# Kernel tuning notes

Measured on AMD Instinct MI355X. Metric: run time of the kernel, lower is better.

Reference implementation:

```python
import jax, jax.numpy as jnp
import numpy as np

N, D, K = 100000, 512, 32
H1, H2 = 512, 256
LN2PI_2 = float(np.log(2.0 * np.pi) / 2.0)


def _glorot(key, shape):
    fan_in, fan_out = shape[0], shape[1]
    limit = np.sqrt(6.0 / (fan_in + fan_out))
    return jax.random.uniform(key, shape, jnp.float32, -limit, limit)


def setup_inputs() -> dict:
    key = jax.random.key(0)
    k0, k1, k2, k3 = jax.random.split(key, 4)
    return {
        "x": jax.random.normal(k0, (N, D), jnp.float32),
        "W1": _glorot(k1, (D, H1)),
        "b1": jnp.zeros((H1,), jnp.float32),
        "W2": _glorot(k2, (H1, H2)),
        "b2": jnp.zeros((H2,), jnp.float32),
        "W3": _glorot(k3, (H2, K)),
        "b3": jnp.zeros((K,), jnp.float32),
    }


def reference(x, W1, b1, W2, b2, W3, b3):
    # instance attention MLP: softplus hiddens, softmax output -> [N, K]
    h = jax.nn.softplus(x @ W1 + b1)
    h = jax.nn.softplus(h @ W2 + b2)
    att = jax.nn.softmax(h @ W3 + b3, axis=-1)

    att_sum = jnp.sum(att, axis=0)  # [K]
    # weighted mean: sum_n x[n,d] * att[n,k] / sum_n att[n,k]  -> [K, D]
    means = (att.T @ x) / att_sum[:, None]
    # weighted variance: E_w[x^2] - mean^2 (algebraic expansion of
    # sum_n (x - mean)^2 * att / sum att, avoids [N,K,D] intermediate)
    ex2 = (att.T @ (x * x)) / att_sum[:, None]  # [K, D]
    vars_ = ex2 - means * means

    # GMM diagonal log-likelihood, expanded to GEMM form:
    inv_v = 1.0 / vars_  # [K, D]
    maha = (x * x) @ inv_v.T - 2.0 * (x @ (means * inv_v).T) \
           + jnp.sum(means * means * inv_v, axis=-1)[None, :]  # [N, K]
    gmm_log = -0.5 * maha - 0.5 * jnp.sum(jnp.log(vars_), axis=-1)[None, :] - D * LN2PI_2
    return gmm_log, vars_
```

## Files before the change

### kernel.cpp

```cpp
#include <hip/hip_runtime.h>
#include <hip/hip_bf16.h>
#include <math.h>

#define NROWS 100000
#define DDIM  512
#define KCL   32
#define H1DIM 512
#define H2DIM 256
#define LN2PI_2 0.9189385332046727f
#define NCHUNK 196
#define NPAD  100352
#define NBLKL 784

typedef __attribute__((ext_vector_type(8))) short short8;
typedef __attribute__((ext_vector_type(4))) short shortx4;
typedef __attribute__((ext_vector_type(4))) float floatx4;

__device__ __forceinline__ float softplus_f(float v) {
    return fmaxf(v, 0.f) + __logf(1.f + __expf(-fabsf(v)));
}

__device__ __forceinline__ unsigned short f2bf_rne(float f) {
    unsigned int u = __float_as_uint(f);
    return (unsigned short)((u + 0x7fffu + ((u >> 16) & 1u)) >> 16);
}

__device__ __forceinline__ float bf2f(short v) {
    return __uint_as_float(((unsigned int)(unsigned short)v) << 16);
}

__device__ __forceinline__ short8 cvt8(float4 a, float4 b) {
    union { unsigned int u[4]; short8 s; } r;
    asm("v_cvt_pk_bf16_f32 %0, %1, %2" : "=v"(r.u[0]) : "v"(a.x), "v"(a.y));
    asm("v_cvt_pk_bf16_f32 %0, %1, %2" : "=v"(r.u[1]) : "v"(a.z), "v"(a.w));
    asm("v_cvt_pk_bf16_f32 %0, %1, %2" : "=v"(r.u[2]) : "v"(b.x), "v"(b.y));
    asm("v_cvt_pk_bf16_f32 %0, %1, %2" : "=v"(r.u[3]) : "v"(b.z), "v"(b.w));
    return r.s;
}

__global__ __launch_bounds__(256) void cvt_weights(
    const float* __restrict__ W1, const float* __restrict__ W2,
    const float* __restrict__ W3, short* __restrict__ W1T,
    short* __restrict__ W2T, short* __restrict__ W3T)
{
    int idx = blockIdx.x * 256 + threadIdx.x;
    const int n1 = DDIM * H1DIM;
    const int n2 = H1DIM * H2DIM;
    const int n3 = H2DIM * KCL;
    if (idx < n1) {
        int n = idx % H1DIM, k = idx / H1DIM;
        W1T[(size_t)n * DDIM + k] = (short)f2bf_rne(W1[idx]);
    } else if (idx < n1 + n2) {
        int rel = idx - n1;
        int n = rel % H2DIM, k = rel / H2DIM;
        W2T[(size_t)n * H1DIM + k] = (short)f2bf_rne(W2[rel]);
    } else if (idx < n1 + n2 + n3) {
        int rel = idx - n1 - n2;
        int n = rel % KCL, k = rel / KCL;
        W3T[(size_t)n * H2DIM + k] = (short)f2bf_rne(W3[rel]);
    }
}

#define LDP 40
__global__ __launch_bounds__(1024, 4) void gemm1_fused(
    const float* __restrict__ x, const short* __restrict__ W1T,
    const float* __restrict__ b1, short* __restrict__ h1,
    short* __restrict__ xb)
{
    __shared__ short As[2][128 * LDP];
    __shared__ short Bs[2][512 * LDP];

    const int tid = threadIdx.x;
    const int lid = tid & 63;
    const int w = tid >> 6;
    const int lm = lid & 15;
    const int lq = lid >> 4;
    const int wrow = (w & 1) * 64;
    const int wcol = (w >> 1) * 64;

    const int row0 = blockIdx.x * 128;

    const int sr = tid >> 2;
    const int sc = (tid & 3) << 3;
    const bool doA = (tid < 512);

    const short* Br0 = W1T + (size_t)sr * DDIM + sc;
    const short* Br1 = W1T + (size_t)(256 + sr) * DDIM + sc;

    int gra = row0 + sr;
    if (gra >= NROWS) gra = NROWS - 1;
    const float* Arf = x + (size_t)gra * DDIM + sc;
    short* xbw = xb + (size_t)gra * DDIM + sc;

    floatx4 acc[4][4];
    #pragma unroll
    for (int i = 0; i < 4; i++)
        #pragma unroll
        for (int j = 0; j < 4; j++)
            acc[i][j] = (floatx4){0.f, 0.f, 0.f, 0.f};

    float4 fa0, fa1;
    short8 pb0, pb1;
    if (doA) {
        fa0 = *(const float4*)Arf;
        fa1 = *(const float4*)(Arf + 4);
    }
    pb0 = *(const short8*)Br0;
    pb1 = *(const short8*)Br1;

    const int nk = DDIM >> 5;
    for (int kt = 0; kt < nk; kt++) {
        const int buf = kt & 1;
        if (doA) {
            short8 cv = cvt8(fa0, fa1);
            *(short8*)&As[buf][sr * LDP + sc] = cv;
            *(short8*)&xbw[kt * 32] = cv;
        }
        *(short8*)&Bs[buf][sr * LDP + sc]         = pb0;
        *(short8*)&Bs[buf][(256 + sr) * LDP + sc] = pb1;
        if (kt + 1 < nk) {
            int ko = (kt + 1) << 5;
            if (doA) {
                fa0 = *(const float4*)(Arf + ko);
                fa1 = *(const float4*)(Arf + ko + 4);
            }
            pb0 = *(const short8*)(Br0 + ko);
            pb1 = *(const short8*)(Br1 + ko);
        }
        __syncthreads();

        short8 a[4], b[4];
        #pragma unroll
        for (int i = 0; i < 4; i++)
            a[i] = *(const short8*)&As[buf][(wrow + i * 16 + lm) * LDP + lq * 8];
        #pragma unroll
        for (int j = 0; j < 4; j++)
            b[j] = *(const short8*)&Bs[buf][(wcol + j * 16 + lm) * LDP + lq * 8];
        #pragma unroll
        for (int i = 0; i < 4; i++)
            #pragma unroll
            for (int j = 0; j < 4; j++)
                acc[i][j] = __builtin_amdgcn_mfma_f32_16x16x32_bf16(
                    a[i], b[j], acc[i][j], 0, 0, 0);
    }

    float bb[4];
    #pragma unroll
    for (int j = 0; j < 4; j++)
        bb[j] = b1[wcol + j * 16 + lm];

    #pragma unroll
    for (int i = 0; i < 4; i++) {
        #pragma unroll
        for (int reg = 0; reg < 4; reg++) {
            int rr = row0 + wrow + i * 16 + lq * 4 + reg;
            if (rr < NROWS) {
                #pragma unroll
                for (int j = 0; j < 4; j++) {
                    int c = wcol + j * 16 + lm;
                    float v = softplus_f(acc[i][j][reg] + bb[j]);
                    h1[(size_t)rr * H1DIM + c] = (short)f2bf_rne(v);
                }
            }
        }
    }
}

__global__ __launch_bounds__(512) void gemm2_logits(
    const short* __restrict__ h1, const short* __restrict__ W2T,
    const float* __restrict__ b2, const short* __restrict__ W3T,
    const float* __restrict__ b3, short* __restrict__ attT,
    float* __restrict__ Patt)
{
    __shared__ __align__(16) short lds[32768];
    __shared__ float red[8][32];

    short* AsB = lds;
    short* BsB = lds + 2 * 128 * LDP;

    const int tid = threadIdx.x;
    const int lid = tid & 63;
    const int w = tid >> 6;
    const int lm = lid & 15;
    const int lq = lid >> 4;
    const int wrow = (w & 1) * 64;
    const int wcol = (w >> 1) * 64;

    const int row0 = blockIdx.x * 128;

    const int sr = tid >> 2;
    const int sc = (tid & 3) << 3;

    int gr = row0 + sr; if (gr >= NROWS) gr = NROWS - 1;
    const short* Ar  = h1  + (size_t)gr * H1DIM + sc;
    const short* Br0 = W2T + (size_t)sr * H1DIM + sc;
    const short* Br1 = W2T + (size_t)(128 + sr) * H1DIM + sc;

    floatx4 acc[4][4];
    #pragma unroll
    for (int i = 0; i < 4; i++)
        #pragma unroll
        for (int j = 0; j < 4; j++)
            acc[i][j] = (floatx4){0.f, 0.f, 0.f, 0.f};

    short8 pa, pb0, pb1;
    pa  = *(const short8*)Ar;
    pb0 = *(const short8*)Br0;
    pb1 = *(const short8*)Br1;

    const int nk = H1DIM >> 5;
    for (int kt = 0; kt < nk; kt++) {
        const int buf = kt & 1;
        *(short8*)&AsB[buf * (128 * LDP) + sr * LDP + sc]         = pa;
        *(short8*)&BsB[buf * (256 * LDP) + sr * LDP + sc]         = pb0;
        *(short8*)&BsB[buf * (256 * LDP) + (128 + sr) * LDP + sc] = pb1;
        if (kt + 1 < nk) {
            int ko = (kt + 1) << 5;
            pa  = *(const short8*)(Ar + ko);
            pb0 = *(const short8*)(Br0 + ko);
            pb1 = *(const short8*)(Br1 + ko);
        }
        __syncthreads();

        short8 a[4], b[4];
        #pragma unroll
        for (int i = 0; i < 4; i++)
            a[i] = *(const short8*)&AsB[buf * (128 * LDP) + (wrow + i * 16 + lm) * LDP + lq * 8];
        #pragma unroll
        for (int j = 0; j < 4; j++)
            b[j] = *(const short8*)&BsB[buf * (256 * LDP) + (wcol + j * 16 + lm) * LDP + lq * 8];
        #pragma unroll
        for (int i = 0; i < 4; i++)
            #pragma unroll
            for (int j = 0; j < 4; j++)
                acc[i][j] = __builtin_amdgcn_mfma_f32_16x16x32_bf16(
                    a[i], b[j], acc[i][j], 0, 0, 0);
    }

    __syncthreads();

    float bb2[4];
    #pragma unroll
    for (int j = 0; j < 4; j++)
        bb2[j] = b2[wcol + j * 16 + lm];
    #pragma unroll
    for (int i = 0; i < 4; i++) {
        #pragma unroll
        for (int reg = 0; reg < 4; reg++) {
            const int r = wrow + i * 16 + lq * 4 + reg;
            const int rx = (r & 7) << 4;
            #pragma unroll
            for (int j = 0; j < 4; j++) {
                const int c = wcol + j * 16 + lm;
                float v = softplus_f(acc[i][j][reg] + bb2[j]);
                *(short*)((char*)lds + ((r * 512 + c * 2) ^ rx)) =
                    (short)f2bf_rne(v);
            }
        }
    }
    __syncthreads();

    short8 bf3[2][8];
    #pragma unroll
    for (int j = 0; j < 2; j++)
        #pragma unroll
        for (int s = 0; s < 8; s++)
            bf3[j][s] = *(const short8*)&W3T[(j * 16 + lm) * H2DIM + s * 32 + lq * 8];

    floatx4 lacc[2];
    lacc[0] = (floatx4){0.f, 0.f, 0.f, 0.f};
    lacc[1] = (floatx4){0.f, 0.f, 0.f, 0.f};
    const int lr = w * 16 + lm;
    const int lrx = (lr & 7) << 4;
    #pragma unroll
    for (int s = 0; s < 8; s++) {
        short8 a0 = *(const short8*)((const char*)lds +
                        ((lr * 512 + s * 64 + lq * 16) ^ lrx));
        lacc[0] = __builtin_amdgcn_mfma_f32_16x16x32_bf16(a0, bf3[0][s], lacc[0], 0, 0, 0);
        lacc[1] = __builtin_amdgcn_mfma_f32_16x16x32_bf16(a0, bf3[1][s], lacc[1], 0, 0, 0);
    }

    const float b3v0 = b3[lm];
    const float b3v1 = b3[16 + lm];
    float p0 = 0.f, p1 = 0.f;
    float e0s[4], e1s[4];
    #pragma unroll
    for (int reg = 0; reg < 4; reg++) {
        const int rg = row0 + w * 16 + lq * 4 + reg;
        float v0 = lacc[0][reg] + b3v0;
        float v1 = lacc[1][reg] + b3v1;
        float m = fmaxf(v0, v1);
        m = fmaxf(m, __shfl_xor(m, 1));
        m = fmaxf(m, __shfl_xor(m, 2));
        m = fmaxf(m, __shfl_xor(m, 4));
        m = fmaxf(m, __shfl_xor(m, 8));
        float e0 = __expf(v0 - m);
        float e1 = __expf(v1 - m);
        float sm = e0 + e1;
        sm += __shfl_xor(sm, 1);
        sm += __shfl_xor(sm, 2);
        sm += __shfl_xor(sm, 4);
        sm += __shfl_xor(sm, 8);
        float inv = 1.f / sm;
        e0 *= inv; e1 *= inv;
        if (rg >= NROWS) { e0 = 0.f; e1 = 0.f; }
        p0 += e0; p1 += e1;
        e0s[reg] = e0; e1s[reg] = e1;
    }
    p0 += __shfl_xor(p0, 16); p0 += __shfl_xor(p0, 32);
    p1 += __shfl_xor(p1, 16); p1 += __shfl_xor(p1, 32);
    if (lq == 0) { red[w][lm] = p0; red[w][16 + lm] = p1; }

    __syncthreads();

    short (*Ts)[136] = (short(*)[136])lds;
    #pragma unroll
    for (int reg = 0; reg < 4; reg++) {
        const int rloc = w * 16 + lq * 4 + reg;
        Ts[lm][rloc]      = (short)f2bf_rne(e0s[reg]);
        Ts[16 + lm][rloc] = (short)f2bf_rne(e1s[reg]);
    }
    __syncthreads();

    if (tid < KCL) {
        float ps = 0.f;
        #pragma unroll
        for (int ww = 0; ww < 8; ww++) ps += red[ww][tid];
        Patt[blockIdx.x * KCL + tid] = ps;
    }

    {
        int rr = tid >> 4;
        int cs = (tid & 15) << 3;
        *(short8*)&attT[(size_t)rr * NPAD + row0 + cs] =
            *(const short8*)&Ts[rr][cs];
    }
}

__global__ __launch_bounds__(256, 4) void stats_mfma(
    const short* __restrict__ xb, const short* __restrict__ attT,
    float* __restrict__ P)
{
    __shared__ short xT[32 * 512];

    const int tid = threadIdx.x;
    const int lane = tid & 63;
    const int lm = lane & 15;
    const int lq = lane >> 4;
    const int w = tid >> 6;
    const int kh = w >> 1;
    const int dh = w & 1;

    const int cblk = blockIdx.x;
    const int dgrp = blockIdx.y;
    const int n0 = cblk * 512;

    short8 afrag[16];
    const short* arow = attT + (size_t)(kh * 16 + lm) * NPAD + n0 + lq * 8;
    #pragma unroll
    for (int s = 0; s < 16; s++)
        afrag[s] = *(const short8*)(arow + s * 32);

    const int c = tid & 31;
    const int rq = tid >> 5;
    const bool full = (n0 + 512 <= NROWS);

    for (int dt = 0; dt < 4; dt++) {
        const int colf = dgrp * 128 + dt * 32 + c;
        __syncthreads();
        if (full) {
            const short* xp = xb + (size_t)n0 * DDIM + colf;
            #pragma unroll 4
            for (int p = 0; p < 16; p++) {
                int rr = p * 32 + rq * 4;
                unsigned int h0 = (unsigned short)xp[(size_t)(rr + 0) * DDIM];
                unsigned int h1 = (unsigned short)xp[(size_t)(rr + 1) * DDIM];
                unsigned int h2 = (unsigned short)xp[(size_t)(rr + 2) * DDIM];
                unsigned int h3 = (unsigned short)xp[(size_t)(rr + 3) * DDIM];
                int boff = (c << 10) + ((rr * 2) ^ ((c & 15) << 4));
                *(uint2*)((char*)xT + boff) =
                    make_uint2(h0 | (h1 << 16), h2 | (h3 << 16));
            }
        } else {
            #pragma unroll 4
            for (int p = 0; p < 16; p++) {
                int rr = p * 32 + rq * 4;
                int g0 = min(n0 + rr + 0, NROWS - 1);
                int g1 = min(n0 + rr + 1, NROWS - 1);
                int g2 = min(n0 + rr + 2, NROWS - 1);
                int g3 = min(n0 + rr + 3, NROWS - 1);
                unsigned int h0 = (unsigned short)xb[(size_t)g0 * DDIM + colf];
                unsigned int h1 = (unsigned short)xb[(size_t)g1 * DDIM + colf];
                unsigned int h2 = (unsigned short)xb[(size_t)g2 * DDIM + colf];
                unsigned int h3 = (unsigned short)xb[(size_t)g3 * DDIM + colf];
                int boff = (c << 10) + ((rr * 2) ^ ((c & 15) << 4));
                *(uint2*)((char*)xT + boff) =
                    make_uint2(h0 | (h1 << 16), h2 | (h3 << 16));
            }
        }
        __syncthreads();

        floatx4 acc1 = (floatx4){0.f, 0.f, 0.f, 0.f};
        floatx4 acc2 = (floatx4){0.f, 0.f, 0.f, 0.f};
        const int rowb = (dh * 16 + lm) << 10;
        #pragma unroll
        for (int s = 0; s < 16; s++) {
            int boff = rowb + ((s * 64 + lq * 16) ^ (lm << 4));
            short8 bx = *(const short8*)((const char*)xT + boff);
            union { short8 s8; unsigned int u[4]; } bq;
            #pragma unroll
            for (int e = 0; e < 4; e++) {
                float f0 = bf2f(bx[2 * e]);
                float f1 = bf2f(bx[2 * e + 1]);
                f0 *= f0; f1 *= f1;
                bq.u[e] = (unsigned int)f2bf_rne(f0) |
                          ((unsigned int)f2bf_rne(f1) << 16);
            }
            acc1 = __builtin_amdgcn_mfma_f32_16x16x32_bf16(
                afrag[s], bx, acc1, 0, 0, 0);
            acc2 = __builtin_amdgcn_mfma_f32_16x16x32_bf16(
                afrag[s], bq.s8, acc2, 0, 0, 0);
        }

        const size_t pbase = (size_t)cblk * 32768 +
                             (size_t)(kh * 16 + lq * 4) * 512 +
                             (size_t)(dgrp * 128 + dt * 32 + dh * 16 + lm);
        #pragma unroll
        for (int reg = 0; reg < 4; reg++) {
            P[pbase + (size_t)reg * 512]         = acc1[reg];
            P[pbase + 16384 + (size_t)reg * 512] = acc2[reg];
        }
    }
}

__global__ __launch_bounds__(256) void stats_reduce(
    const float* __restrict__ P, const float* __restrict__ Patt,
    float* __restrict__ S12, float* __restrict__ att_sum)
{
    int e = blockIdx.x * 256 + threadIdx.x;
    float sum = 0.f;
    for (int cc = 0; cc < NCHUNK; cc++)
        sum += P[(size_t)cc * 32768 + e];
    S12[e] = sum;

    if (blockIdx.x == 0 && threadIdx.x < KCL) {
        float as = 0.f;
        for (int cc = 0; cc < NBLKL; cc++) as += Patt[cc * KCL + threadIdx.x];
        att_sum[threadIdx.x] = as;
    }
}

__global__ __launch_bounds__(256) void finalize_stats(
    const float* __restrict__ S12, const float* __restrict__ att_sum,
    short* __restrict__ Bp, float* __restrict__ konst,
    float* __restrict__ vars_out)
{
    int k = blockIdx.x;
    int tid = threadIdx.x;
    __shared__ float red[256];

    float inv_as = 1.f / att_sum[k];
    float csum = 0.f, lsum = 0.f;
    for (int d = tid; d < DDIM; d += 256) {
        float mean = S12[k * DDIM + d] * inv_as;
        float ex2  = S12[KCL * DDIM + k * DDIM + d] * inv_as;
        float var  = ex2 - mean * mean;
        vars_out[k * DDIM + d] = var;
        float iv = 1.f / var;
        Bp[(size_t)k * 1024 + d]       = (short)f2bf_rne(-0.5f * iv);
        Bp[(size_t)k * 1024 + 512 + d] = (short)f2bf_rne(mean * iv);
        csum += mean * mean * iv;
        lsum += logf(var);
    }
    red[tid] = csum;
    __syncthreads();
    for (int s = 128; s > 0; s >>= 1) {
        if (tid < s) red[tid] += red[tid + s];
        __syncthreads();
    }
    float ctot = red[0];
    __syncthreads();
    red[tid] = lsum;
    __syncthreads();
    for (int s = 128; s > 0; s >>= 1) {
        if (tid < s) red[tid] += red[tid + s];
        __syncthreads();
    }
    if (tid == 0)
        konst[k] = -0.5f * ctot - 0.5f * red[0] - DDIM * LN2PI_2;
}

#define LDG 40
__global__ __launch_bounds__(256) void gmm_out_mfma(
    const short* __restrict__ xb, const short* __restrict__ Bp,
    const float* __restrict__ konst, float* __restrict__ out)
{
    __shared__ short As_sq[128 * LDG];
    __shared__ short As_x[128 * LDG];

    const int tid = threadIdx.x;
    const int lane = tid & 63;
    const int lm = lane & 15;
    const int lq = lane >> 4;
    const int wid = tid >> 6;
    const int row0 = blockIdx.x * 128;

    floatx4 acc[2][2];
    #pragma unroll
    for (int i = 0; i < 2; i++)
        #pragma unroll
        for (int j = 0; j < 2; j++)
            acc[i][j] = (floatx4){0.f, 0.f, 0.f, 0.f};

    int rrh[4], segh[4], grh[4];
    bool okh[4];
    #pragma unroll
    for (int h = 0; h < 4; h++) {
        int u = tid + h * 256;
        rrh[h] = u >> 3;
        segh[h] = (u & 7) << 2;
        int gr = row0 + rrh[h];
        okh[h] = (gr < NROWS);
        grh[h] = okh[h] ? gr : 0;
    }

    shortx4 pf[4];
    #pragma unroll
    for (int h = 0; h < 4; h++) {
        shortx4 v = (shortx4){0, 0, 0, 0};
        if (okh[h]) v = *(const shortx4*)&xb[(size_t)grh[h] * DDIM + segh[h]];
        pf[h] = v;
    }

    for (int dt = 0; dt < 16; dt++) {
        __syncthreads();
        #pragma unroll
        for (int h = 0; h < 4; h++) {
            shortx4 sx = pf[h];
            shortx4 sq;
            #pragma unroll
            for (int e = 0; e < 4; e++) {
                float f = bf2f(sx[e]);
                sq[e] = (short)f2bf_rne(f * f);
            }
            *(shortx4*)&As_x[rrh[h] * LDG + segh[h]]  = sx;
            *(shortx4*)&As_sq[rrh[h] * LDG + segh[h]] = sq;
        }
        if (dt + 1 < 16) {
            #pragma unroll
            for (int h = 0; h < 4; h++) {
                shortx4 v = (shortx4){0, 0, 0, 0};
                if (okh[h])
                    v = *(const shortx4*)&xb[(size_t)grh[h] * DDIM +
                                             (dt + 1) * 32 + segh[h]];
                pf[h] = v;
            }
        }
        __syncthreads();

        short8 a_sq[2], a_x[2], b_sq[2], b_x[2];
        #pragma unroll
        for (int i = 0; i < 2; i++) {
            int off = (wid * 32 + i * 16 + lm) * LDG + lq * 8;
            a_sq[i] = *(const short8*)&As_sq[off];
            a_x[i]  = *(const short8*)&As_x[off];
        }
        #pragma unroll
        for (int j = 0; j < 2; j++) {
            const size_t bo = (size_t)(j * 16 + lm) * 1024 + dt * 32 + lq * 8;
            b_sq[j] = *(const short8*)&Bp[bo];
            b_x[j]  = *(const short8*)&Bp[bo + 512];
        }
        #pragma unroll
        for (int i = 0; i < 2; i++)
            #pragma unroll
            for (int j = 0; j < 2; j++) {
                acc[i][j] = __builtin_amdgcn_mfma_f32_16x16x32_bf16(
                    a_sq[i], b_sq[j], acc[i][j], 0, 0, 0);
                acc[i][j] = __builtin_amdgcn_mfma_f32_16x16x32_bf16(
                    a_x[i], b_x[j], acc[i][j], 0, 0, 0);
            }
    }

    float kst[2];
    kst[0] = konst[lm];
    kst[1] = konst[16 + lm];

    #pragma unroll
    for (int i = 0; i < 2; i++) {
        #pragma unroll
        for (int reg = 0; reg < 4; reg++) {
            int rr = row0 + wid * 32 + i * 16 + lq * 4 + reg;
            if (rr < NROWS) {
                out[(size_t)rr * KCL + lm]      = acc[i][0][reg] + kst[0];
                out[(size_t)rr * KCL + 16 + lm] = acc[i][1][reg] + kst[1];
            }
        }
    }
}

extern "C" void kernel_launch(void* const* d_in, const int* in_sizes, int n_in,
                              void* d_out, int out_size, void* d_ws, size_t ws_size,
                              hipStream_t stream)
{
    const float* x  = (const float*)d_in[0];
    const float* W1 = (const float*)d_in[1];
    const float* b1 = (const float*)d_in[2];
    const float* W2 = (const float*)d_in[3];
    const float* b2 = (const float*)d_in[4];
    const float* W3 = (const float*)d_in[5];
    const float* b3 = (const float*)d_in[6];
    float* out = (float*)d_out;

    short* h1b     = (short*)d_ws;
    float* h2      = (float*)(h1b + (size_t)NROWS * H1DIM);
    float* att     = h2 + (size_t)NROWS * H2DIM;
    float* P       = att + (size_t)NROWS * KCL;
    float* PattOld = P + (size_t)NCHUNK * 32768;
    float* S12     = PattOld + NCHUNK * KCL;
    float* att_sum = S12 + 2 * KCL * DDIM;
    short* Bp      = (short*)(att_sum + KCL);
    float* konst   = (float*)(Bp + KCL * 1024);
    (void)ws_size; (void)in_sizes; (void)n_in; (void)out_size; (void)PattOld;

    short* xb = (short*)h2;
    short* attT  = (short*)att;
    float* PattN = (float*)(attT + (size_t)KCL * NPAD);
    short* W1T = (short*)P;
    short* W2T = W1T + H1DIM * DDIM;
    short* W3T = W2T + H2DIM * H1DIM;

    cvt_weights<<<dim3(1568), 256, 0, stream>>>(W1, W2, W3, W1T, W2T, W3T);

    int mblocks = (NROWS + 127) / 128;

    gemm1_fused<<<dim3(mblocks), 1024, 0, stream>>>(x, W1T, b1, h1b, xb);
    gemm2_logits<<<dim3(NBLKL), 512, 0, stream>>>(
        h1b, W2T, b2, W3T, b3, attT, PattN);
    stats_mfma<<<dim3(NCHUNK, 4), 256, 0, stream>>>(xb, attT, P);
    stats_reduce<<<dim3(128), 256, 0, stream>>>(P, PattN, S12, att_sum);
    finalize_stats<<<dim3(KCL), 256, 0, stream>>>(
        S12, att_sum, Bp, konst, out + (size_t)NROWS * KCL);
    gmm_out_mfma<<<dim3(mblocks), 256, 0, stream>>>(
        xb, Bp, konst, out);
}
```

Before: 586.6 us.

## Load W1 fragments directly from global in gemm1, shrink row tile to 64

The first GEMM no longer stages W1 through shared memory. Each wave now reads its B fragments straight from global memory, relying on L2/cache reuse of the small bf16 W1. The block tile drops from 128 rows and 1024 threads to 64 rows and 512 threads, so LDS use is much smaller and more blocks can be resident. The trade-off is more global and L2 traffic for weights: every block re-reads all of W1, and each wave reads its fragments uncoalesced across rows.

```diff
diff --git a/kernel.cpp b/kernel.cpp
--- a/kernel.cpp
+++ b/kernel.cpp
@@ -11,6 +11,7 @@
 #define NCHUNK 196
 #define NPAD  100352
 #define NBLKL 784
+#define NBLK1 1563
 
 typedef __attribute__((ext_vector_type(8))) short short8;
 typedef __attribute__((ext_vector_type(4))) short shortx4;
@@ -62,36 +63,37 @@
 }
 
 #define LDP 40
-__global__ __launch_bounds__(1024, 4) void gemm1_fused(
+__global__ __launch_bounds__(512, 4) void gemm1_fused(
     const float* __restrict__ x, const short* __restrict__ W1T,
     const float* __restrict__ b1, short* __restrict__ h1,
     short* __restrict__ xb)
 {
-    __shared__ short As[2][128 * LDP];
-    __shared__ short Bs[2][512 * LDP];
+    __shared__ short As[2][64 * LDP];
 
     const int tid = threadIdx.x;
     const int lid = tid & 63;
     const int w = tid >> 6;
     const int lm = lid & 15;
     const int lq = lid >> 4;
-    const int wrow = (w & 1) * 64;
-    const int wcol = (w >> 1) * 64;
-
-    const int row0 = blockIdx.x * 128;
+    const int wcol = w * 64;
+
+    const int row0 = blockIdx.x * 64;
 
     const int sr = tid >> 2;
     const int sc = (tid & 3) << 3;
-    const bool doA = (tid < 512);
-
-    const short* Br0 = W1T + (size_t)sr * DDIM + sc;
-    const short* Br1 = W1T + (size_t)(256 + sr) * DDIM + sc;
-
-    int gra = row0 + sr;
+    const bool doA = (tid < 256);
+
+    int gra = row0 + (sr & 63);
+    const bool aval = (gra < NROWS);
     if (gra >= NROWS) gra = NROWS - 1;
     const float* Arf = x + (size_t)gra * DDIM + sc;
     short* xbw = xb + (size_t)gra * DDIM + sc;
 
+    const short* Wb0 = W1T + (size_t)(wcol +  0 + lm) * DDIM + lq * 8;
+    const short* Wb1 = W1T + (size_t)(wcol + 16 + lm) * DDIM + lq * 8;
+    const short* Wb2 = W1T + (size_t)(wcol + 32 + lm) * DDIM + lq * 8;
+    const short* Wb3 = W1T + (size_t)(wcol + 48 + lm) * DDIM + lq * 8;
+
     floatx4 acc[4][4];
     #pragma unroll
     for (int i = 0; i < 4; i++)
@@ -100,13 +102,10 @@
             acc[i][j] = (floatx4){0.f, 0.f, 0.f, 0.f};
 
     float4 fa0, fa1;
-    short8 pb0, pb1;
     if (doA) {
         fa0 = *(const float4*)Arf;
         fa1 = *(const float4*)(Arf + 4);
     }
-    pb0 = *(const short8*)Br0;
-    pb1 = *(const short8*)Br1;
 
     const int nk = DDIM >> 5;
     for (int kt = 0; kt < nk; kt++) {
@@ -114,28 +113,29 @@
         if (doA) {
             short8 cv = cvt8(fa0, fa1);
             *(short8*)&As[buf][sr * LDP + sc] = cv;
-            *(short8*)&xbw[kt * 32] = cv;
-        }
-        *(short8*)&Bs[buf][sr * LDP + sc]         = pb0;
-        *(short8*)&Bs[buf][(256 + sr) * LDP + sc] = pb1;
+            if (aval) *(short8*)&xbw[kt * 32] = cv;
+        }
         if (kt + 1 < nk) {
-            int ko = (kt + 1) << 5;
             if (doA) {
+                int ko = (kt + 1) << 5;
                 fa0 = *(const float4*)(Arf + ko);
                 fa1 = *(const float4*)(Arf + ko + 4);
             }
-            pb0 = *(const short8*)(Br0 + ko);
-            pb1 = *(const short8*)(Br1 + ko);
-        }
-        __syncthreads();
-
-        short8 a[4], b[4];
+        }
+        short8 b[4];
+        {
+            const int ko = kt * 32;
+            b[0] = *(const short8*)(Wb0 + ko);
+            b[1] = *(const short8*)(Wb1 + ko);
+            b[2] = *(const short8*)(Wb2 + ko);
+            b[3] = *(const short8*)(Wb3 + ko);
+        }
+        __syncthreads();
+
+        short8 a[4];
         #pragma unroll
         for (int i = 0; i < 4; i++)
-            a[i] = *(const short8*)&As[buf][(wrow + i * 16 + lm) * LDP + lq * 8];
-        #pragma unroll
-        for (int j = 0; j < 4; j++)
-            b[j] = *(const short8*)&Bs[buf][(wcol + j * 16 + lm) * LDP + lq * 8];
+            a[i] = *(const short8*)&As[buf][(i * 16 + lm) * LDP + lq * 8];
         #pragma unroll
         for (int i = 0; i < 4; i++)
             #pragma unroll
@@ -153,7 +153,7 @@
     for (int i = 0; i < 4; i++) {
         #pragma unroll
         for (int reg = 0; reg < 4; reg++) {
-            int rr = row0 + wrow + i * 16 + lq * 4 + reg;
+            int rr = row0 + i * 16 + lq * 4 + reg;
             if (rr < NROWS) {
                 #pragma unroll
                 for (int j = 0; j < 4; j++) {
@@ -632,15 +632,13 @@
 
     cvt_weights<<<dim3(1568), 256, 0, stream>>>(W1, W2, W3, W1T, W2T, W3T);
 
-    int mblocks = (NROWS + 127) / 128;
-
-    gemm1_fused<<<dim3(mblocks), 1024, 0, stream>>>(x, W1T, b1, h1b, xb);
+    gemm1_fused<<<dim3(NBLK1), 512, 0, stream>>>(x, W1T, b1, h1b, xb);
     gemm2_logits<<<dim3(NBLKL), 512, 0, stream>>>(
         h1b, W2T, b2, W3T, b3, attT, PattN);
     stats_mfma<<<dim3(NCHUNK, 4), 256, 0, stream>>>(xb, attT, P);
     stats_reduce<<<dim3(128), 256, 0, stream>>>(P, PattN, S12, att_sum);
     finalize_stats<<<dim3(KCL), 256, 0, stream>>>(
         S12, att_sum, Bp, konst, out + (size_t)NROWS * KCL);
-    gmm_out_mfma<<<dim3(mblocks), 256, 0, stream>>>(
+    gmm_out_mfma<<<dim3((NROWS + 127) / 128), 256, 0, stream>>>(
         xb, Bp, konst, out);
 }
```

After: 643.6 us. +9.7%, slower.
